# Kernel optimization log

Hardware: AMD Instinct MI355X
Metric: run time of the kernel (lower is better)

## Reference

```python
import jax, jax.numpy as jnp
import numpy as np
from jax import lax

V, E, H, SEQ = 50257, 512, 512, 2048
TAGS, START, STOP = 12, 10, 11
NEG = -10000.0


def _lstm_dir(x, Wih, Whh, bih, bhh, reverse):
    # x: [T, in], Wih: [4H, in], Whh: [4H, H] (torch gate order i,f,g,o)
    h0 = jnp.zeros((Whh.shape[1],), x.dtype)
    c0 = jnp.zeros((Whh.shape[1],), x.dtype)
    b = bih + bhh

    def step(carry, xt):
        h, c = carry
        gates = Wih @ xt + Whh @ h + b  # [4H]
        i, f, g, o = jnp.split(gates, 4)
        c = jax.nn.sigmoid(f) * c + jax.nn.sigmoid(i) * jnp.tanh(g)
        h = jax.nn.sigmoid(o) * jnp.tanh(c)
        return (h, c), h

    _, hs = lax.scan(step, (h0, c0), x, reverse=reverse)
    return hs  # [T, H]


def _bilstm_layer(x, Wih, Whh, bih, bhh):
    # stacked params: leading dim 2 = (fwd, bwd)
    fwd = _lstm_dir(x, Wih[0], Whh[0], bih[0], bhh[0], False)
    bwd = _lstm_dir(x, Wih[1], Whh[1], bih[1], bhh[1], True)
    return jnp.concatenate([fwd, bwd], axis=-1)  # [T, 2H]


def _viterbi(feats, transitions):
    # feats: [T, TAGS]; transitions[next, prev]
    init = jnp.full((TAGS,), NEG, feats.dtype).at[START].set(0.0)

    def step(fv, feat):
        scores = fv[None, :] + transitions  # [next, prev]
        bptr = jnp.argmax(scores, axis=1)
        fv_new = jnp.max(scores, axis=1) + feat
        return fv_new, bptr

    fv, bptrs = lax.scan(step, init, feats)
    terminal = fv + transitions[STOP]
    best_last = jnp.argmax(terminal)
    path_score = terminal[best_last]

    def back(tag, bp):
        prev = bp[tag]
        return prev, prev

    _, ys = lax.scan(back, best_last, bptrs, reverse=True)
    # ys[t] = path[t-1]; ys[0] = START (dropped); append best_last
    best_path = jnp.concatenate([ys[1:], best_last[None]])
    return path_score, best_path


def setup_inputs() -> dict:
    key = jax.random.key(0)
    ks = jax.random.split(key, 16)
    s = lambda *sh: 1.0 / np.sqrt(H)
    inp = {
        "sentence": jax.random.randint(ks[0], (SEQ,), 0, V),
        "emb": jax.random.normal(ks[1], (V, E), jnp.float32),
        "Wih0": jax.random.uniform(ks[2], (2, 4 * H, E), jnp.float32, -s(), s()),
        "Whh0": jax.random.uniform(ks[3], (2, 4 * H, H), jnp.float32, -s(), s()),
        "bih0": jax.random.uniform(ks[4], (2, 4 * H), jnp.float32, -s(), s()),
        "bhh0": jax.random.uniform(ks[5], (2, 4 * H), jnp.float32, -s(), s()),
        "Wih1": jax.random.uniform(ks[6], (2, 4 * H, 2 * H), jnp.float32, -s(), s()),
        "Whh1": jax.random.uniform(ks[7], (2, 4 * H, H), jnp.float32, -s(), s()),
        "bih1": jax.random.uniform(ks[8], (2, 4 * H), jnp.float32, -s(), s()),
        "bhh1": jax.random.uniform(ks[9], (2, 4 * H), jnp.float32, -s(), s()),
        "W_tag": jax.random.uniform(ks[10], (TAGS, 2 * H), jnp.float32, -0.1, 0.1),
        "b_tag": jnp.zeros((TAGS,), jnp.float32),
    }
    trans = jax.random.normal(ks[11], (TAGS, TAGS), jnp.float32)
    trans = trans.at[START, :].set(NEG).at[:, STOP].set(NEG)
    inp["transitions"] = trans
    return inp


def reference(sentence, emb, Wih0, Whh0, bih0, bhh0, Wih1, Whh1, bih1, bhh1, W_tag, b_tag, transitions):
    x = emb[sentence]  # [T, E]  (dropout identity in eval)
    x = _bilstm_layer(x, Wih0, Whh0, bih0, bhh0)
    x = _bilstm_layer(x, Wih1, Whh1, bih1, bhh1)
    feats = x @ W_tag.T + b_tag  # [T, TAGS]
    path_score, best_path = _viterbi(feats, transitions)
    return path_score, best_path
```

## Files before the change

### kernel.cpp

```cpp
#include <hip/hip_runtime.h>
#include <math.h>

#define SEQ 2048
#define EMB_D 512
#define HID 512
#define NTAGS 12
#define START_TAG 10
#define STOP_TAG 11
#define NEGV (-10000.0f)
#define POISON 0xAAAAAAAAu

__device__ __forceinline__ float sigf(float x) { return 1.0f / (1.0f + expf(-x)); }

__global__ void k_embed(const int* __restrict__ sent, const float* __restrict__ emb,
                        float* __restrict__ x0) {
    int t = blockIdx.x;
    int tid = threadIdx.x;
    int row = sent[t];
    const float4* src = (const float4*)(emb + (size_t)row * EMB_D);
    float4* dst = (float4*)(x0 + (size_t)t * EMB_D);
    dst[tid] = src[tid];
}

#define GBM 128
#define GBN 128
#define GBK 16
#define GLD 132

__global__ __launch_bounds__(256) void k_gemm(
    const float* __restrict__ Af, const float* __restrict__ Ab,
    const float* __restrict__ B,
    const float* __restrict__ biasA, const float* __restrict__ biasB,
    float* __restrict__ C, int K) {
    const int N = 2048;
    int dir = blockIdx.z;
    const float* Bd = B + (size_t)dir * N * K;
    const float* bA = biasA + dir * N;
    const float* bB = biasB + dir * N;
    float* Cd = C + (size_t)dir * 2048 * N;
    int m0 = blockIdx.y * GBM, n0 = blockIdx.x * GBN;

    __shared__ float As[GBK * GLD];
    __shared__ float Bs[GBK * GLD];

    int tid = threadIdx.x;
    int lrow = tid >> 1;
    int lk = (tid & 1) * 8;
    int tx = tid & 15, ty = tid >> 4;

    float acc[8][8] = {};

    for (int kt = 0; kt < K; kt += GBK) {
        {
            int m = m0 + lrow;
            const float* base = (kt < 512) ? (Af + (size_t)m * 512 + kt)
                                           : (Ab + (size_t)m * 512 + (kt - 512));
            float4 v0 = *(const float4*)(base + lk);
            float4 v1 = *(const float4*)(base + lk + 4);
            As[(lk + 0) * GLD + lrow] = v0.x;
            As[(lk + 1) * GLD + lrow] = v0.y;
            As[(lk + 2) * GLD + lrow] = v0.z;
            As[(lk + 3) * GLD + lrow] = v0.w;
            As[(lk + 4) * GLD + lrow] = v1.x;
            As[(lk + 5) * GLD + lrow] = v1.y;
            As[(lk + 6) * GLD + lrow] = v1.z;
            As[(lk + 7) * GLD + lrow] = v1.w;
        }
        {
            int n = n0 + lrow;
            const float* base = Bd + (size_t)n * K + kt;
            float4 v0 = *(const float4*)(base + lk);
            float4 v1 = *(const float4*)(base + lk + 4);
            Bs[(lk + 0) * GLD + lrow] = v0.x;
            Bs[(lk + 1) * GLD + lrow] = v0.y;
            Bs[(lk + 2) * GLD + lrow] = v0.z;
            Bs[(lk + 3) * GLD + lrow] = v0.w;
            Bs[(lk + 4) * GLD + lrow] = v1.x;
            Bs[(lk + 5) * GLD + lrow] = v1.y;
            Bs[(lk + 6) * GLD + lrow] = v1.z;
            Bs[(lk + 7) * GLD + lrow] = v1.w;
        }
        __syncthreads();
#pragma unroll
        for (int kk = 0; kk < GBK; ++kk) {
            float4 a0 = *(const float4*)&As[kk * GLD + ty * 8];
            float4 a1 = *(const float4*)&As[kk * GLD + ty * 8 + 4];
            float4 b0 = *(const float4*)&Bs[kk * GLD + tx * 8];
            float4 b1 = *(const float4*)&Bs[kk * GLD + tx * 8 + 4];
            float av[8] = {a0.x, a0.y, a0.z, a0.w, a1.x, a1.y, a1.z, a1.w};
            float bv[8] = {b0.x, b0.y, b0.z, b0.w, b1.x, b1.y, b1.z, b1.w};
#pragma unroll
            for (int i = 0; i < 8; ++i)
#pragma unroll
                for (int j = 0; j < 8; ++j) acc[i][j] += av[i] * bv[j];
        }
        __syncthreads();
    }
#pragma unroll
    for (int i = 0; i < 8; ++i) {
        int m = m0 + ty * 8 + i;
#pragma unroll
        for (int j = 0; j < 8; ++j) {
            int n = n0 + tx * 8 + j;
            Cd[(size_t)m * N + n] = acc[i][j] + bA[n] + bB[n];
        }
    }
}

#define HPAD 132

__global__ __launch_bounds__(256, 1) void k_lstm(
    const float* __restrict__ Whh,
    const float* __restrict__ Gi,
    float* __restrict__ hstore)
{
    int wg = blockIdx.x;
    int dir = wg >> 5;
    int slice = wg & 31;
    int u_base = slice * 16;
    int tid = threadIdx.x;

    const float* Whh_d = Whh + (size_t)dir * 2048 * 512;
    const float* Gi_d = Gi + (size_t)dir * 2048 * 2048;
    float* h_d = hstore + (size_t)dir * 2048 * 512;

    int rl = tid >> 2;
    int kp = tid & 3;
    int gg = rl >> 4;
    int uu = rl & 15;
    int r = gg * 512 + u_base + uu;

    float w[128];
    {
        const float* wsrc = Whh_d + (size_t)r * 512 + kp * 128;
#pragma unroll
        for (int j = 0; j < 128; j += 4) {
            float4 v = *(const float4*)(wsrc + j);
            w[j] = v.x; w[j + 1] = v.y; w[j + 2] = v.z; w[j + 3] = v.w;
        }
    }

    __shared__ __align__(16) float hlds[4 * HPAD];
    __shared__ float gdot[64];
    float c_reg = 0.0f;

    int sec = tid >> 6;
    int soff = (tid & 63) * 2;
    float* hstage = hlds + sec * HPAD + soff;

    float gi = 0.f;
    {
        int t0 = dir ? 2047 : 0;
        if (kp == 0) gi = Gi_d[(size_t)t0 * 2048 + r];
    }

    for (int it = 0; it < 2048; ++it) {
        int t = dir ? (2047 - it) : it;

        if (it == 0) {
            hstage[0] = 0.f;
            hstage[1] = 0.f;
        } else {
            int tprev = dir ? (t + 1) : (t - 1);
            const unsigned long long* src =
                (const unsigned long long*)(h_d + (size_t)tprev * 512) + tid;
            unsigned long long v;
            do {
                v = __hip_atomic_load(src, __ATOMIC_RELAXED, __HIP_MEMORY_SCOPE_AGENT);
            } while ((unsigned)v == POISON || (unsigned)(v >> 32) == POISON);
            hstage[0] = __uint_as_float((unsigned)v);
            hstage[1] = __uint_as_float((unsigned)(v >> 32));
        }
        __syncthreads();

        float gi_next = 0.f;
        if (kp == 0 && it + 1 < 2048) {
            int tn = dir ? (t - 1) : (t + 1);
            gi_next = Gi_d[(size_t)tn * 2048 + r];
        }

        float p = 0.f;
        const float4* h4 = (const float4*)(hlds + kp * HPAD);
#pragma unroll
        for (int j4 = 0; j4 < 32; ++j4) {
            float4 hv = h4[j4];
            p += w[4 * j4 + 0] * hv.x;
            p += w[4 * j4 + 1] * hv.y;
            p += w[4 * j4 + 2] * hv.z;
            p += w[4 * j4 + 3] * hv.w;
        }
        p += __shfl_xor(p, 1);
        p += __shfl_xor(p, 2);
        if (kp == 0) {
            float v = p + gi;
            gdot[rl] = (gg == 2) ? tanhf(v) : sigf(v);
        }
        __syncthreads();

        if (tid < 16) {
            float iv = gdot[0 * 16 + tid];
            float fv = gdot[1 * 16 + tid];
            float gv = gdot[2 * 16 + tid];
            float ov = gdot[3 * 16 + tid];
            float c = fv * c_reg + iv * gv;
            float h = ov * tanhf(c);
            c_reg = c;
            __hip_atomic_store(h_d + (size_t)t * 512 + u_base + tid, h,
                               __ATOMIC_RELAXED, __HIP_MEMORY_SCOPE_AGENT);
        }
        gi = gi_next;
    }
}

__global__ __launch_bounds__(64) void k_feats(
    const float* __restrict__ h1,
    const float* __restrict__ Wt,
    const float* __restrict__ bt,
    float* __restrict__ feats)
{
    int t = blockIdx.x;
    int lane = threadIdx.x;
    __shared__ __align__(16) float xl[1024];
    const float4* hf = (const float4*)(h1 + (size_t)t * 512);
    const float4* hb = (const float4*)(h1 + (size_t)(2048 + t) * 512);
    ((float4*)xl)[lane] = hf[lane];
    ((float4*)xl)[lane + 64] = hf[lane + 64];
    ((float4*)xl)[128 + lane] = hb[lane];
    ((float4*)xl)[128 + lane + 64] = hb[lane + 64];
    __syncthreads();
    for (int tag = 0; tag < NTAGS; ++tag) {
        const float* wrow = Wt + tag * 1024;
        float s = 0.f;
        for (int k = lane; k < 1024; k += 64) s += xl[k] * wrow[k];
#pragma unroll
        for (int off = 32; off; off >>= 1) s += __shfl_xor(s, off);
        if (lane == 0) feats[t * NTAGS + tag] = s + bt[tag];
    }
}

__global__ __launch_bounds__(64) void k_viterbi(
    const float* __restrict__ feats, const float* __restrict__ trans,
    float* __restrict__ out) {
    __shared__ float fv[2][NTAGS];
    __shared__ unsigned char bp[SEQ * NTAGS];
    __shared__ float featbuf[256 * NTAGS];
    __shared__ float term[NTAGS];
    int lane = threadIdx.x;

    float tr[NTAGS];
    if (lane < NTAGS) {
#pragma unroll
        for (int p = 0; p < NTAGS; ++p) tr[p] = trans[lane * NTAGS + p];
        fv[0][lane] = (lane == START_TAG) ? 0.f : NEGV;
    }
    __syncthreads();

    int cur = 0;
    for (int tc = 0; tc < SEQ; tc += 256) {
        for (int i = lane; i < 256 * NTAGS; i += 64) featbuf[i] = feats[tc * NTAGS + i];
        __syncthreads();
        for (int tt = 0; tt < 256; ++tt) {
            int t = tc + tt;
            if (lane < NTAGS) {
                float best = fv[cur][0] + tr[0];
                int bi = 0;
#pragma unroll
                for (int p = 1; p < NTAGS; ++p) {
                    float s = fv[cur][p] + tr[p];
                    if (s > best) { best = s; bi = p; }
                }
                bp[t * NTAGS + lane] = (unsigned char)bi;
                fv[cur ^ 1][lane] = best + featbuf[tt * NTAGS + lane];
            }
            cur ^= 1;
            __syncthreads();
        }
    }

    if (lane < NTAGS) term[lane] = fv[cur][lane] + trans[STOP_TAG * NTAGS + lane];
    __syncthreads();
    if (lane == 0) {
        float best = term[0];
        int bi = 0;
        for (int p = 1; p < NTAGS; ++p) {
            if (term[p] > best) { best = term[p]; bi = p; }
        }
        out[0] = best;
        int tag = bi;
        out[1 + (SEQ - 1)] = (float)tag;
        for (int t = SEQ - 1; t >= 1; --t) {
            tag = bp[t * NTAGS + tag];
            out[t] = (float)tag;
        }
    }
}

extern "C" void kernel_launch(void* const* d_in, const int* in_sizes, int n_in,
                              void* d_out, int out_size, void* d_ws, size_t ws_size,
                              hipStream_t stream) {
    const int* sent = (const int*)d_in[0];
    const float* emb = (const float*)d_in[1];
    const float* Wih0 = (const float*)d_in[2];
    const float* Whh0 = (const float*)d_in[3];
    const float* bih0 = (const float*)d_in[4];
    const float* bhh0 = (const float*)d_in[5];
    const float* Wih1 = (const float*)d_in[6];
    const float* Whh1 = (const float*)d_in[7];
    const float* bih1 = (const float*)d_in[8];
    const float* bhh1 = (const float*)d_in[9];
    const float* Wtag = (const float*)d_in[10];
    const float* btag = (const float*)d_in[11];
    const float* trans = (const float*)d_in[12];
    float* out = (float*)d_out;

    char* ws = (char*)d_ws;
    size_t off = 0;
    auto alloc = [&](size_t bytes) {
        void* p = ws + off;
        off += (bytes + 255) & ~(size_t)255;
        return p;
    };
    float* x0 = (float*)alloc(2048ull * 512 * 4);
    float* Gi = (float*)alloc(2ull * 2048 * 2048 * 4);
    float* h0 = (float*)alloc(2ull * 2048 * 512 * 4);
    float* h1 = (float*)alloc(2ull * 2048 * 512 * 4);
    float* feats = (float*)alloc(2048ull * NTAGS * 4);

    hipMemsetAsync(h0, 0xAA, 2ull * 2048 * 512 * 4, stream);
    hipMemsetAsync(h1, 0xAA, 2ull * 2048 * 512 * 4, stream);

    k_embed<<<2048, 128, 0, stream>>>(sent, emb, x0);

    dim3 gg(16, 16, 2);
    k_gemm<<<gg, 256, 0, stream>>>(x0, x0, Wih0, bih0, bhh0, Gi, 512);
    k_lstm<<<64, 256, 0, stream>>>(Whh0, Gi, h0);
    k_gemm<<<gg, 256, 0, stream>>>(h0, h0 + 2048ull * 512, Wih1, bih1, bhh1, Gi, 1024);
    k_lstm<<<64, 256, 0, stream>>>(Whh1, Gi, h1);
    k_feats<<<2048, 64, 0, stream>>>(h1, Wtag, btag, feats);
    k_viterbi<<<1, 64, 0, stream>>>(feats, trans, out);
}
```

Before: 8.879 ms.

## Spread LSTM blocks across XCDs and poll hidden state with sc0 loads

The recurrent LSTM kernel now launches 256 blocks and keeps only those with blockIdx%8 in {0,1}. Assuming round-robin XCD assignment, this places each direction's 32 blocks on a single XCD so they exchange hidden state through a shared L2. Polling uses inline-asm global loads with sc0, falling back to agent-scope atomics after several tries. Each block writes its own h slice straight into LDS and skips polling for it. The change relies on an undocumented block-to-XCD mapping and adds a duplicate store plus 192 empty blocks.

```diff
diff --git a/kernel.cpp b/kernel.cpp
--- a/kernel.cpp
+++ b/kernel.cpp
@@ -11,6 +11,19 @@
 #define POISON 0xAAAAAAAAu
 
 __device__ __forceinline__ float sigf(float x) { return 1.0f / (1.0f + expf(-x)); }
+
+__device__ __forceinline__ unsigned long long ld_sc0_u64(const float* p) {
+    unsigned long long ap = (unsigned long long)p;
+    unsigned long long v;
+    asm volatile("global_load_dwordx2 %0, %1, off sc0\n\ts_waitcnt vmcnt(0)"
+                 : "=v"(v)
+                 : "v"(ap));
+    return v;
+}
+__device__ __forceinline__ void st_sc0_f32(float* p, float x) {
+    unsigned long long ap = (unsigned long long)p;
+    asm volatile("global_store_dword %0, %1, off sc0" ::"v"(ap), "v"(x));
+}
 
 __global__ void k_embed(const int* __restrict__ sent, const float* __restrict__ emb,
                         float* __restrict__ x0) {
@@ -114,9 +127,11 @@
     const float* __restrict__ Gi,
     float* __restrict__ hstore)
 {
-    int wg = blockIdx.x;
-    int dir = wg >> 5;
-    int slice = wg & 31;
+    int bid = blockIdx.x;
+    int xsel = bid & 7;
+    if (xsel >= 2) return;
+    int dir = xsel;
+    int slice = bid >> 3;
     int u_base = slice * 16;
     int tid = threadIdx.x;
 
@@ -147,6 +162,7 @@
     int sec = tid >> 6;
     int soff = (tid & 63) * 2;
     float* hstage = hlds + sec * HPAD + soff;
+    bool own_pair = (tid >= slice * 8) && (tid < slice * 8 + 8);
 
     float gi = 0.f;
     {
@@ -160,14 +176,28 @@
         if (it == 0) {
             hstage[0] = 0.f;
             hstage[1] = 0.f;
-        } else {
+        } else if (!own_pair) {
             int tprev = dir ? (t + 1) : (t - 1);
-            const unsigned long long* src =
-                (const unsigned long long*)(h_d + (size_t)tprev * 512) + tid;
+            const float* srcf = h_d + (size_t)tprev * 512 + 2 * tid;
             unsigned long long v;
-            do {
-                v = __hip_atomic_load(src, __ATOMIC_RELAXED, __HIP_MEMORY_SCOPE_AGENT);
-            } while ((unsigned)v == POISON || (unsigned)(v >> 32) == POISON);
+            int tries = 0;
+            for (;;) {
+                v = ld_sc0_u64(srcf);
+                if ((unsigned)v != POISON && (unsigned)(v >> 32) != POISON) break;
+                if (++tries >= 6) {
+                    const unsigned long long* src = (const unsigned long long*)srcf;
+                    for (;;) {
+                        v = __hip_atomic_load(src, __ATOMIC_RELAXED,
+                                              __HIP_MEMORY_SCOPE_AGENT);
+                        if ((unsigned)v != POISON && (unsigned)(v >> 32) != POISON)
+                            break;
+                        v = ld_sc0_u64(srcf);
+                        if ((unsigned)v != POISON && (unsigned)(v >> 32) != POISON)
+                            break;
+                    }
+                    break;
+                }
+            }
             hstage[0] = __uint_as_float((unsigned)v);
             hstage[1] = __uint_as_float((unsigned)(v >> 32));
         }
@@ -205,7 +235,10 @@
             float c = fv * c_reg + iv * gv;
             float h = ov * tanhf(c);
             c_reg = c;
-            __hip_atomic_store(h_d + (size_t)t * 512 + u_base + tid, h,
+            int g = u_base + tid;
+            hlds[(g >> 7) * HPAD + (g & 127)] = h;
+            st_sc0_f32(h_d + (size_t)t * 512 + g, h);
+            __hip_atomic_store(h_d + (size_t)t * 512 + g, h,
                                __ATOMIC_RELAXED, __HIP_MEMORY_SCOPE_AGENT);
         }
         gi = gi_next;
@@ -333,9 +366,9 @@
 
     dim3 gg(16, 16, 2);
     k_gemm<<<gg, 256, 0, stream>>>(x0, x0, Wih0, bih0, bhh0, Gi, 512);
-    k_lstm<<<64, 256, 0, stream>>>(Whh0, Gi, h0);
+    k_lstm<<<256, 256, 0, stream>>>(Whh0, Gi, h0);
     k_gemm<<<gg, 256, 0, stream>>>(h0, h0 + 2048ull * 512, Wih1, bih1, bhh1, Gi, 1024);
-    k_lstm<<<64, 256, 0, stream>>>(Whh1, Gi, h1);
+    k_lstm<<<256, 256, 0, stream>>>(Whh1, Gi, h1);
     k_feats<<<2048, 64, 0, stream>>>(h1, Wtag, btag, feats);
     k_viterbi<<<1, 64, 0, stream>>>(feats, trans, out);
 }
```

Measured after the change: 11.79 ms. 32.7% more time.

## Fuse layer-0 LSTM with layer-1 input GEMM using poison-flag readiness polling

Applied to the files above, without the earlier changes.

Layer 0's LSTM recurrence and layer 1's input-projection GEMM now run in one persistent launch. The GEMM tiles spin until the needed h0 rows no longer hold the poison value, then load them with atomic 64-bit reads. The goal is to hide the layer-1 GEMM behind the serial layer-0 recurrence and save one kernel boundary. The risks are that polling blocks share CUs with the latency-critical LSTM blocks, and that raising launch bounds to three blocks per CU could pressure registers in the LSTM body.

```diff
diff --git a/kernel.cpp b/kernel.cpp
--- a/kernel.cpp
+++ b/kernel.cpp
@@ -11,6 +11,14 @@
 #define POISON 0xAAAAAAAAu
 
 __device__ __forceinline__ float sigf(float x) { return 1.0f / (1.0f + expf(-x)); }
+
+__device__ __forceinline__ unsigned long long ald64(const float* p) {
+    return __hip_atomic_load((const unsigned long long*)p, __ATOMIC_RELAXED,
+                             __HIP_MEMORY_SCOPE_AGENT);
+}
+__device__ __forceinline__ bool pois2(unsigned long long x) {
+    return (unsigned)x == POISON || (unsigned)(x >> 32) == POISON;
+}
 
 __global__ void k_embed(const int* __restrict__ sent, const float* __restrict__ emb,
                         float* __restrict__ x0) {
@@ -109,12 +117,15 @@
 
 #define HPAD 132
 
-__global__ __launch_bounds__(256, 1) void k_lstm(
+__device__ __forceinline__ void lstm_body(
+    int wg,
     const float* __restrict__ Whh,
     const float* __restrict__ Gi,
     float* __restrict__ hstore)
 {
-    int wg = blockIdx.x;
+    __shared__ __align__(16) float hlds[4 * HPAD];
+    __shared__ float gdot[64];
+
     int dir = wg >> 5;
     int slice = wg & 31;
     int u_base = slice * 16;
@@ -140,8 +151,6 @@
         }
     }
 
-    __shared__ __align__(16) float hlds[4 * HPAD];
-    __shared__ float gdot[64];
     float c_reg = 0.0f;
 
     int sec = tid >> 6;
@@ -212,12 +221,131 @@
     }
 }
 
+__global__ __launch_bounds__(256, 1) void k_lstm(
+    const float* __restrict__ Whh, const float* __restrict__ Gi,
+    float* __restrict__ hstore) {
+    lstm_body(blockIdx.x, Whh, Gi, hstore);
+}
+
+__device__ void gemm1_body(int bt, const float* h0, const float* Wih1,
+                           const float* bih1, const float* bhh1, float* Gi) {
+    __shared__ float As[GBK * GLD];
+    __shared__ float Bs[GBK * GLD];
+    __shared__ int ready;
+
+    int dir = bt >> 8;
+    int rem = bt & 255;
+    int tm = rem >> 4, tn = rem & 15;
+    int tid = threadIdx.x;
+
+    const float* h0f = h0;
+    const float* h0b = h0 + 2048ull * 512;
+    const float* Bd = Wih1 + (size_t)dir * 2048 * 1024;
+    const float* bA = bih1 + dir * 2048;
+    const float* bB = bhh1 + dir * 2048;
+    float* Cd = Gi + (size_t)dir * 2048 * 2048;
+    int m0 = tm * GBM, n0 = tn * GBN;
+
+    if (tid == 0) ready = 0;
+    __syncthreads();
+    for (;;) {
+        if (tid < 64) {
+            int s = tid & 31;
+            const float* base = (tid < 32) ? (h0f + (size_t)(m0 + 127) * 512)
+                                           : (h0b + (size_t)m0 * 512);
+            float v = __hip_atomic_load(base + 16 * s + 15, __ATOMIC_RELAXED,
+                                        __HIP_MEMORY_SCOPE_AGENT);
+            unsigned long long m = __ballot(__float_as_uint(v) != POISON);
+            if (tid == 0 && m == ~0ull) ready = 1;
+        }
+        __syncthreads();
+        if (ready) break;
+        __builtin_amdgcn_s_sleep(64);
+        __syncthreads();
+    }
+
+    int lrow = tid >> 1;
+    int lk = (tid & 1) * 8;
+    int tx = tid & 15, ty = tid >> 4;
+
+    float acc[8][8] = {};
+
+    for (int kt = 0; kt < 1024; kt += GBK) {
+        {
+            int m = m0 + lrow;
+            const float* base = (kt < 512) ? (h0f + (size_t)m * 512 + kt)
+                                           : (h0b + (size_t)m * 512 + (kt - 512));
+            const float* p = base + lk;
+            unsigned long long q0, q1, q2, q3;
+            for (;;) {
+                q0 = ald64(p + 0);
+                q1 = ald64(p + 2);
+                q2 = ald64(p + 4);
+                q3 = ald64(p + 6);
+                if (!(pois2(q0) | pois2(q1) | pois2(q2) | pois2(q3))) break;
+            }
+            As[(lk + 0) * GLD + lrow] = __uint_as_float((unsigned)q0);
+            As[(lk + 1) * GLD + lrow] = __uint_as_float((unsigned)(q0 >> 32));
+            As[(lk + 2) * GLD + lrow] = __uint_as_float((unsigned)q1);
+            As[(lk + 3) * GLD + lrow] = __uint_as_float((unsigned)(q1 >> 32));
+            As[(lk + 4) * GLD + lrow] = __uint_as_float((unsigned)q2);
+            As[(lk + 5) * GLD + lrow] = __uint_as_float((unsigned)(q2 >> 32));
+            As[(lk + 6) * GLD + lrow] = __uint_as_float((unsigned)q3);
+            As[(lk + 7) * GLD + lrow] = __uint_as_float((unsigned)(q3 >> 32));
+        }
+        {
+            int n = n0 + lrow;
+            const float* base = Bd + (size_t)n * 1024 + kt;
+            float4 v0 = *(const float4*)(base + lk);
+            float4 v1 = *(const float4*)(base + lk + 4);
+            Bs[(lk + 0) * GLD + lrow] = v0.x;
+            Bs[(lk + 1) * GLD + lrow] = v0.y;
+            Bs[(lk + 2) * GLD + lrow] = v0.z;
+            Bs[(lk + 3) * GLD + lrow] = v0.w;
+            Bs[(lk + 4) * GLD + lrow] = v1.x;
+            Bs[(lk + 5) * GLD + lrow] = v1.y;
+            Bs[(lk + 6) * GLD + lrow] = v1.z;
+            Bs[(lk + 7) * GLD + lrow] = v1.w;
+        }
+        __syncthreads();
+#pragma unroll
+        for (int kk = 0; kk < GBK; ++kk) {
+            float4 a0 = *(const float4*)&As[kk * GLD + ty * 8];
+            float4 a1 = *(const float4*)&As[kk * GLD + ty * 8 + 4];
+            float4 b0 = *(const float4*)&Bs[kk * GLD + tx * 8];
+            float4 b1 = *(const float4*)&Bs[kk * GLD + tx * 8 + 4];
+            float av[8] = {a0.x, a0.y, a0.z, a0.w, a1.x, a1.y, a1.z, a1.w};
+            float bv[8] = {b0.x, b0.y, b0.z, b0.w, b1.x, b1.y, b1.z, b1.w};
+#pragma unroll
+            for (int i = 0; i < 8; ++i)
+#pragma unroll
+                for (int j = 0; j < 8; ++j) acc[i][j] += av[i] * bv[j];
+        }
+        __syncthreads();
+    }
+#pragma unroll
+    for (int i = 0; i < 8; ++i) {
+        int m = m0 + ty * 8 + i;
+#pragma unroll
+        for (int j = 0; j < 8; ++j) {
+            int n = n0 + tx * 8 + j;
+            Cd[(size_t)m * 2048 + n] = acc[i][j] + bA[n] + bB[n];
+        }
+    }
+}
+
+__global__ __launch_bounds__(256, 3) void k_fused(
+    const float* Whh0, float* Gi, float* h0,
+    const float* Wih1, const float* bih1, const float* bhh1) {
+    if (blockIdx.x < 64)
+        lstm_body(blockIdx.x, Whh0, Gi, h0);
+    else
+        gemm1_body(blockIdx.x - 64, h0, Wih1, bih1, bhh1, Gi);
+}
+
 __global__ __launch_bounds__(64) void k_feats(
-    const float* __restrict__ h1,
-    const float* __restrict__ Wt,
-    const float* __restrict__ bt,
-    float* __restrict__ feats)
-{
+    const float* __restrict__ h1, const float* __restrict__ Wt,
+    const float* __restrict__ bt, float* __restrict__ feats) {
     int t = blockIdx.x;
     int lane = threadIdx.x;
     __shared__ __align__(16) float xl[1024];
@@ -331,10 +459,8 @@
 
     k_embed<<<2048, 128, 0, stream>>>(sent, emb, x0);
 
-    dim3 gg(16, 16, 2);
-    k_gemm<<<gg, 256, 0, stream>>>(x0, x0, Wih0, bih0, bhh0, Gi, 512);
-    k_lstm<<<64, 256, 0, stream>>>(Whh0, Gi, h0);
-    k_gemm<<<gg, 256, 0, stream>>>(h0, h0 + 2048ull * 512, Wih1, bih1, bhh1, Gi, 1024);
+    k_gemm<<<dim3(16, 16, 2), 256, 0, stream>>>(x0, x0, Wih0, bih0, bhh0, Gi, 512);
+    k_fused<<<576, 256, 0, stream>>>(Whh0, Gi, h0, Wih1, bih1, bhh1);
     k_lstm<<<64, 256, 0, stream>>>(Whh1, Gi, h1);
     k_feats<<<2048, 64, 0, stream>>>(h1, Wtag, btag, feats);
     k_viterbi<<<1, 64, 0, stream>>>(feats, trans, out);
```

New measurement: 9.028 ms. About the same (+1.7%).
